# Kernel tuning notes

Measured on AMD Instinct MI355X. Metric: run time of the kernel, lower is better.

## Reference

```python
import jax, jax.numpy as jnp
import numpy as np

BITS = 4
GROUPSIZE = 128
IN_FEATURES = 4096
OUT_FEATURES = 11008
N_GROUPS = IN_FEATURES // GROUPSIZE  # 32
MASK = (1 << BITS) - 1  # 15


def setup_inputs() -> dict:
    key = jax.random.key(0)
    ks = jax.random.split(key, 5)
    x = jax.random.normal(ks[0], (2, 2048, IN_FEATURES), dtype=jnp.float32)
    qweight = jax.random.randint(ks[1], (IN_FEATURES // 8, OUT_FEATURES), 0, 2**31 - 1, dtype=jnp.int32)
    qzeros = jax.random.randint(ks[2], (N_GROUPS, OUT_FEATURES // 8), 0, 2**31 - 1, dtype=jnp.int32)
    scales = jax.random.uniform(ks[3], (N_GROUPS, OUT_FEATURES), dtype=jnp.float16)
    bias = jax.random.normal(ks[4], (OUT_FEATURES,), dtype=jnp.float32)
    return {"x": x, "qweight": qweight, "qzeros": qzeros, "scales": scales, "bias": bias}


def _dequant(qweight, qzeros, scales):
    # wf = [0, 4, 8, ..., 28]: bit offsets of the 8 int4 nibbles in each int32
    wf = jnp.arange(0, 32, BITS, dtype=jnp.int32)
    # unpack weights: [IN//8, OUT] -> [IN//8, 8, OUT] -> [N_GROUPS, GROUPSIZE, OUT]
    w = (qweight[:, None, :] >> wf[None, :, None]) & MASK
    w = w.reshape(N_GROUPS, GROUPSIZE, OUT_FEATURES).astype(jnp.float32)
    # unpack zeros: [NG, OUT//8] -> [NG, OUT//8, 8] -> [NG, 1, OUT]
    z = (qzeros[:, :, None] >> wf[None, None, :]) & MASK
    z = z.reshape(N_GROUPS, 1, OUT_FEATURES).astype(jnp.float32)
    s = scales.astype(jnp.float32)[:, None, :]  # [NG, 1, OUT]
    # scales * w - scales * z, per group; fused elementwise
    return (s * (w - z)).reshape(IN_FEATURES, OUT_FEATURES)


def reference(x, qweight, qzeros, scales, bias):
    W = _dequant(qweight, qzeros, scales)  # [IN, OUT] fp32
    out = jnp.matmul(x.astype(jnp.float32), W) + bias
    return out
```

## Files before the change

### kernel.cpp

```cpp
#include <hip/hip_runtime.h>
#include <hip/hip_fp16.h>

#define K_DIM 4096
#define N_DIM 11008
#define NZ8   1376
#define BM    256
#define BN    256
#define NT_N  43
#define NKT   64
#define ATB   32768

typedef _Float16 f16x8 __attribute__((ext_vector_type(8)));
typedef float    f32x4 __attribute__((ext_vector_type(4)));

#define SB()    __builtin_amdgcn_sched_barrier(0)
#define BAR()   __builtin_amdgcn_s_barrier()
#define VMW(N)  do { asm volatile("s_waitcnt vmcnt(" #N ")" ::: "memory"); SB(); } while (0)
#define LGKM0() do { asm volatile("s_waitcnt lgkmcnt(0)" ::: "memory"); SB(); } while (0)

__device__ __forceinline__ f16x8 dq8(unsigned q, __half2 scp, __half2 nzp)
{
    const unsigned mu = 0xE400E400u;
    const __half2 m1024 = *(const __half2*)&mu;
    union { __half2 h2[4]; f16x8 v; } p;
#pragma unroll
    for (int d = 0; d < 4; ++d) {
        unsigned t = ((q >> (4 * d)) & 0x000F000Fu) | 0x64006400u;
        p.h2[d] = __hfma2(__hadd2(*(const __half2*)&t, m1024), scp, nzp);
    }
    return p.v;
}

__global__ __launch_bounds__(256)
void r15_xcvt(const float* __restrict__ x, __half* __restrict__ xh, int nchunks)
{
    int c = blockIdx.x * 256 + threadIdx.x;
    const int stride = gridDim.x * 256;
    for (; c < nchunks; c += stride) {
        const int row = c & 255;
        const int sl  = (c >> 8) & 3;
        const int kh  = (c >> 10) & 1;
        const int tl  = c >> 11;
        const int mt  = tl >> 6;
        const int kt  = tl & 63;
        const size_t gm = (size_t)mt * 256 + row;
        const int kb = kt * 64 + kh * 32 + sl * 8;
        const float4 f0 = *(const float4*)(x + gm * K_DIM + kb);
        const float4 f1 = *(const float4*)(x + gm * K_DIM + kb + 4);
        union { __half2 h2[4]; int4 v; } p;
        p.h2[0] = __floats2half2_rn(f0.x, f1.x);
        p.h2[1] = __floats2half2_rn(f0.y, f1.y);
        p.h2[2] = __floats2half2_rn(f0.z, f1.z);
        p.h2[3] = __floats2half2_rn(f0.w, f1.w);
        ((int4*)xh)[c] = p.v;
    }
}

#define ISSUE_Q8(D0,D1,D2,D3,D4,D5,D6,D7) do { \
    asm volatile( \
        "global_load_dword %0, %8, off\n\t" \
        "global_load_dword %1, %8, off offset:64\n\t" \
        "global_load_dword %2, %8, off offset:128\n\t" \
        "global_load_dword %3, %8, off offset:192\n\t" \
        "global_load_dword %4, %9, off\n\t" \
        "global_load_dword %5, %9, off offset:64\n\t" \
        "global_load_dword %6, %9, off offset:128\n\t" \
        "global_load_dword %7, %9, off offset:192" \
        : "=&v"(D0), "=&v"(D1), "=&v"(D2), "=&v"(D3), \
          "=&v"(D4), "=&v"(D5), "=&v"(D6), "=&v"(D7) \
        : "v"(qp0), "v"(qp1) : "memory"); \
    qp0 += 8 * N_DIM; qp1 += 8 * N_DIM; \
} while (0)

#define ISSUE_SZ() do { \
    asm volatile( \
        "global_load_dword %0, %8, off\n\t" \
        "global_load_dword %1, %8, off offset:64\n\t" \
        "global_load_dword %2, %8, off offset:128\n\t" \
        "global_load_dword %3, %8, off offset:192\n\t" \
        "global_load_dword %4, %9, off\n\t" \
        "global_load_dword %5, %9, off offset:8\n\t" \
        "global_load_dword %6, %9, off offset:16\n\t" \
        "global_load_dword %7, %9, off offset:24" \
        : "=&v"(sS0), "=&v"(sS1), "=&v"(sS2), "=&v"(sS3), \
          "=&v"(sZ0), "=&v"(sZ1), "=&v"(sZ2), "=&v"(sZ3) \
        : "v"(sp), "v"(zp) : "memory"); \
    sp += N_DIM; zp += NZ8; \
} while (0)

#define ISSUE_A(BUFP, T) do { \
    const char* _s = agp + (size_t)(T) * ATB; \
    _Pragma("unroll") for (int j = 0; j < 4; ++j) \
        __builtin_amdgcn_global_load_lds((const unsigned int*)(_s + j * 8192), \
            (unsigned int*)((BUFP) + j * 8192 + tid * 16), 16, 0, 0); \
} while (0)

#define FRAGS(ARp, KH) do { \
    _Pragma("unroll") for (int m = 0; m < 8; ++m) \
        af[m] = *(const f16x8*)((ARp) + (KH) * 16384 + aOff + m * 256); \
} while (0)

#define DQ4(Q0,Q1,Q2,Q3) do { \
    bf[0] = dq8(Q0, scp0, nzp0); bf[1] = dq8(Q1, scp1, nzp1); \
    bf[2] = dq8(Q2, scp2, nzp2); bf[3] = dq8(Q3, scp3, nzp3); \
} while (0)

#define MFMA32() do { \
    __builtin_amdgcn_s_setprio(1); \
    _Pragma("unroll") for (int m = 0; m < 8; ++m) \
        _Pragma("unroll") for (int n = 0; n < 4; ++n) \
            acc[m][n] = __builtin_amdgcn_mfma_f32_16x16x32_f16(af[m], bf[n], acc[m][n], 0, 0, 0); \
    __builtin_amdgcn_s_setprio(0); \
    SB(); \
} while (0)

#define CVT_S() do { \
    const float _s0 = __uint_as_float(sS0), _s1 = __uint_as_float(sS1); \
    const float _s2 = __uint_as_float(sS2), _s3 = __uint_as_float(sS3); \
    const __half _h0 = __float2half_rn(_s0), _h1 = __float2half_rn(_s1); \
    const __half _h2 = __float2half_rn(_s2), _h3 = __float2half_rn(_s3); \
    scp0 = __half2(_h0, _h0); scp1 = __half2(_h1, _h1); \
    scp2 = __half2(_h2, _h2); scp3 = __half2(_h3, _h3); \
    const __half _n0 = __float2half_rn(-_s0 * (float)((sZ0 >> sh4) & 15u)); \
    const __half _n1 = __float2half_rn(-_s1 * (float)((sZ1 >> sh4) & 15u)); \
    const __half _n2 = __float2half_rn(-_s2 * (float)((sZ2 >> sh4) & 15u)); \
    const __half _n3 = __float2half_rn(-_s3 * (float)((sZ3 >> sh4) & 15u)); \
    nzp0 = __half2(_n0, _n0); nzp1 = __half2(_n1, _n1); \
    nzp2 = __half2(_n2, _n2); nzp3 = __half2(_n3, _n3); \
} while (0)

__global__ __launch_bounds__(512, 2)
void r15_gemm(const __half* __restrict__ xh,
              const int*   __restrict__ qweight,
              const int*   __restrict__ qzeros,
              const float* __restrict__ scales,
              const float* __restrict__ bias,
              float* __restrict__ out)
{
    __shared__ __align__(16) unsigned char A0s[ATB], A1s[ATB];

    const int tid  = threadIdx.x;
    const int lane = tid & 63;
    const int wid  = tid >> 6;
    const int wr   = (wid >> 2) * 128;
    const int wc   = (wid & 3) * 64;

    int bid = blockIdx.x;
    const int cpx = gridDim.x >> 3;
    bid = (bid & 7) * cpx + (bid >> 3);
    const int bm0 = (bid / NT_N) * BM;
    const int bn0 = (bid % NT_N) * BN;

    const int frow = lane & 15, kb8 = lane >> 4;
    const int ngl2 = bn0 + wc + frow;
    const int sh4  = (ngl2 & 7) * 4;
    const int aOff = kb8 * 4096 + (wr + frow) * 16;

    const char* agp = (const char*)xh + ((size_t)(bm0 >> 8) * NKT) * ATB + tid * 16;

    const int*   qp0 = qweight + (size_t)kb8 * N_DIM + ngl2;
    const int*   qp1 = qweight + (size_t)(kb8 + 4) * N_DIM + ngl2;
    const float* sp  = scales + (size_t)N_DIM + ngl2;
    const int*   zp  = qzeros + (size_t)NZ8 + (ngl2 >> 3);

    unsigned char *aR = A0s, *aW = A1s;

    f32x4 acc[8][4];
#pragma unroll
    for (int m = 0; m < 8; ++m)
#pragma unroll
        for (int n = 0; n < 4; ++n)
            acc[m][n] = (f32x4){0.f, 0.f, 0.f, 0.f};
    f16x8 af[8], bf[4];
    __half2 scp0, scp1, scp2, scp3, nzp0, nzp1, nzp2, nzp3;
    unsigned qa0, qa1, qa2, qa3, qa4, qa5, qa6, qa7;
    unsigned qb0, qb1, qb2, qb3, qb4, qb5, qb6, qb7;
    unsigned sS0, sS1, sS2, sS3, sZ0, sZ1, sZ2, sZ3;

    sS0 = __float_as_uint(scales[ngl2]);
    sS1 = __float_as_uint(scales[ngl2 + 16]);
    sS2 = __float_as_uint(scales[ngl2 + 32]);
    sS3 = __float_as_uint(scales[ngl2 + 48]);
    sZ0 = (unsigned)qzeros[(ngl2 >> 3) + 0];
    sZ1 = (unsigned)qzeros[(ngl2 >> 3) + 2];
    sZ2 = (unsigned)qzeros[(ngl2 >> 3) + 4];
    sZ3 = (unsigned)qzeros[(ngl2 >> 3) + 6];
    asm volatile("" : "+v"(sS0), "+v"(sS1), "+v"(sS2), "+v"(sS3),
                      "+v"(sZ0), "+v"(sZ1), "+v"(sZ2), "+v"(sZ3));
    VMW(0);
    ISSUE_Q8(qa0, qa1, qa2, qa3, qa4, qa5, qa6, qa7);
    ISSUE_A(aR, 0);
    ISSUE_Q8(qb0, qb1, qb2, qb3, qb4, qb5, qb6, qb7);
    ISSUE_A(aW, 1);
    VMW(12);
    BAR();

    for (int u = 0; u < 31; ++u) {
        const int t0 = 2 * u;
        CVT_S();
        FRAGS(aR, 0); DQ4(qa0, qa1, qa2, qa3); LGKM0(); MFMA32();
        FRAGS(aR, 1); DQ4(qa4, qa5, qa6, qa7);
        ISSUE_Q8(qa0, qa1, qa2, qa3, qa4, qa5, qa6, qa7);
        ISSUE_SZ();
        LGKM0(); MFMA32();
        VMW(16);
        BAR(); SB();
        { unsigned char* tp = aR; aR = aW; aW = tp; }
        ISSUE_A(aW, t0 + 2);
        FRAGS(aR, 0); DQ4(qb0, qb1, qb2, qb3); LGKM0(); MFMA32();
        FRAGS(aR, 1); DQ4(qb4, qb5, qb6, qb7);
        ISSUE_Q8(qb0, qb1, qb2, qb3, qb4, qb5, qb6, qb7);
        LGKM0(); MFMA32();
        VMW(8);
        BAR(); SB();
        { unsigned char* tp = aR; aR = aW; aW = tp; }
        ISSUE_A(aW, t0 + 3);
    }

    CVT_S();
    FRAGS(aR, 0); DQ4(qa0, qa1, qa2, qa3); LGKM0(); MFMA32();
    FRAGS(aR, 1); DQ4(qa4, qa5, qa6, qa7); LGKM0(); MFMA32();
    VMW(0);
    BAR(); SB();
    { unsigned char* tp = aR; aR = aW; aW = tp; }
    FRAGS(aR, 0); DQ4(qb0, qb1, qb2, qb3); LGKM0(); MFMA32();
    FRAGS(aR, 1); DQ4(qb4, qb5, qb6, qb7); LGKM0(); MFMA32();

    const int crow0 = (lane >> 4) << 2, ccol = lane & 15;
#pragma unroll
    for (int n = 0; n < 4; ++n) {
        const int col = bn0 + wc + n * 16 + ccol;
        const float bv = bias[col];
#pragma unroll
        for (int m = 0; m < 8; ++m) {
            const int row = bm0 + wr + m * 16 + crow0;
#pragma unroll
            for (int j = 0; j < 4; ++j)
                out[(size_t)(row + j) * N_DIM + col] = acc[m][n][j] + bv;
        }
    }
}

typedef __bf16 bf16x8 __attribute__((ext_vector_type(8)));

__global__ __launch_bounds__(256, 2)
void r15_fb(const float* __restrict__ x,
            const int*   __restrict__ qweight,
            const int*   __restrict__ qzeros,
            const float* __restrict__ scales,
            const float* __restrict__ bias,
            float* __restrict__ out)
{
    __shared__ __align__(16) unsigned char Asm[128 * 64 * 2];
    __shared__ __align__(16) unsigned char Bsm[128 * 64 * 2];
    const int tid = threadIdx.x, lane = tid & 63, wv = tid >> 6;
    const int wr = (wv >> 1) * 64, wc = (wv & 1) * 64;
    int bid = blockIdx.x;
    const int cpx = gridDim.x >> 3;
    bid = (bid & 7) * cpx + (bid >> 3);
    const int bm0 = (bid / 86) * 128, bn0 = (bid % 86) * 128;
    const int ar = tid >> 4, ac4 = tid & 15;
    const float* xp = x + (size_t)(bm0 + ar) * K_DIM + ac4 * 4;
    unsigned char* aw = Asm + ar * 128 + ((ac4 * 8) ^ ((ar & 7) << 4));
    const int bnn = tid & 127, bk8q = tid >> 7, ngl = bn0 + bnn;
    const int* qwp = qweight + (size_t)bk8q * N_DIM + ngl;
    unsigned char* bw = Bsm + bnn * 128;
    const int bsw = bnn & 7;
    const int frow = lane & 15, kb8 = lane >> 4, fsw = frow & 7;
    f32x4 acc[4][4];
#pragma unroll
    for (int m = 0; m < 4; ++m)
#pragma unroll
        for (int n = 0; n < 4; ++n) acc[m][n] = (f32x4){0.f, 0.f, 0.f, 0.f};
    float sc = 0.f, nsz = 0.f;
    for (int kt = 0; kt < K_DIM / 64; ++kt) {
        const int k0 = kt * 64;
        if ((k0 & 127) == 0) {
            const int g = k0 >> 7;
            sc = scales[(size_t)g * N_DIM + ngl];
            const unsigned zq = (unsigned)qzeros[(size_t)g * NZ8 + (ngl >> 3)];
            nsz = -sc * (float)((zq >> ((ngl & 7) * 4)) & 15u);
        }
#pragma unroll
        for (int i = 0; i < 8; ++i) {
            const float4 v = *(const float4*)(xp + (size_t)i * 16 * K_DIM + k0);
            union { __bf16 h[4]; unsigned long long u; } p;
            p.h[0] = (__bf16)v.x; p.h[1] = (__bf16)v.y;
            p.h[2] = (__bf16)v.z; p.h[3] = (__bf16)v.w;
            *(unsigned long long*)(aw + i * 16 * 128) = p.u;
        }
#pragma unroll
        for (int i = 0; i < 4; ++i) {
            const int k8 = 2 * i + bk8q;
            const unsigned q = (unsigned)qwp[(size_t)(kt * 8 + 2 * i) * N_DIM];
            union { __bf16 h[8]; bf16x8 v8; } p;
#pragma unroll
            for (int j = 0; j < 8; ++j)
                p.h[j] = (__bf16)__builtin_fmaf(sc, (float)((q >> (4 * j)) & 15u), nsz);
            *(bf16x8*)(bw + ((k8 ^ bsw) << 4)) = p.v8;
        }
        __syncthreads();
#pragma unroll
        for (int kh = 0; kh < 2; ++kh) {
            const int ksl = (kh << 2) + kb8;
            bf16x8 a2[4], b2[4];
#pragma unroll
            for (int m = 0; m < 4; ++m)
                a2[m] = *(const bf16x8*)(Asm + (wr + m * 16 + frow) * 128 + ((ksl ^ fsw) << 4));
#pragma unroll
            for (int n = 0; n < 4; ++n)
                b2[n] = *(const bf16x8*)(Bsm + (wc + n * 16 + frow) * 128 + ((ksl ^ fsw) << 4));
#pragma unroll
            for (int m = 0; m < 4; ++m)
#pragma unroll
                for (int n = 0; n < 4; ++n)
                    acc[m][n] = __builtin_amdgcn_mfma_f32_16x16x32_bf16(a2[m], b2[n], acc[m][n], 0, 0, 0);
        }
        __syncthreads();
    }
    const int crow0 = (lane >> 4) << 2, ccol = lane & 15;
#pragma unroll
    for (int n = 0; n < 4; ++n) {
        const int col = bn0 + wc + n * 16 + ccol;
        const float bv = bias[col];
#pragma unroll
        for (int m = 0; m < 4; ++m) {
            const int row = bm0 + wr + m * 16 + crow0;
#pragma unroll
            for (int j = 0; j < 4; ++j)
                out[(size_t)(row + j) * N_DIM + col] = acc[m][n][j] + bv;
        }
    }
}

extern "C" void kernel_launch(void* const* d_in, const int* in_sizes, int n_in,
                              void* d_out, int out_size, void* d_ws, size_t ws_size,
                              hipStream_t stream)
{
    const float* x   = (const float*)d_in[0];
    const int*   qw  = (const int*)d_in[1];
    const int*   qz  = (const int*)d_in[2];
    const float* scl = (const float*)d_in[3];
    const float* bs  = (const float*)d_in[4];
    float* out = (float*)d_out;

    const int M = in_sizes[0] / K_DIM;
    const size_t xh_bytes = (size_t)M * K_DIM * 2;

    if (ws_size >= xh_bytes) {
        __half* xh = (__half*)d_ws;
        const int nchunks = M * K_DIM / 8;
        hipLaunchKernelGGL(r15_xcvt, dim3(2048), dim3(256), 0, stream, x, xh, nchunks);
        dim3 grid((M / BM) * NT_N);
        hipLaunchKernelGGL(r15_gemm, grid, dim3(512), 0, stream,
                           xh, qw, qz, scl, bs, out);
    } else {
        dim3 grid((M / 128) * 86);
        hipLaunchKernelGGL(r15_fb, grid, dim3(256), 0, stream,
                           x, qw, qz, scl, bs, out);
    }
}
```

Measured before the change: 386.2 us.

## Switch GEMM to 32x32x16 MFMA with k-sliced A fragments and pipelined LDS reads

Replaces the 16x16x32 MFMA tiling with 32x32x16 MFMAs, so each wave holds 4x2 accumulators of 16 floats instead of 8x4 of 4. The x fp16 staging layout, the qweight/scale/zero load pattern and the dequant per lane change to match, and each lane now needs only two scale/zero pairs. A-fragment LDS reads are split into four k-slices and double-buffered across register sets with partial lgkmcnt waits, so LDS latency overlaps MFMA issue. The aim is fewer MFMA instructions, less dequant work per lane and fewer stalls on LDS, at the cost of a more intricate schedule and output row mapping.

```diff
diff --git a/kernel.cpp b/kernel.cpp
--- a/kernel.cpp
+++ b/kernel.cpp
@@ -10,13 +10,13 @@
 #define NKT   64
 #define ATB   32768
 
-typedef _Float16 f16x8 __attribute__((ext_vector_type(8)));
-typedef float    f32x4 __attribute__((ext_vector_type(4)));
-
-#define SB()    __builtin_amdgcn_sched_barrier(0)
-#define BAR()   __builtin_amdgcn_s_barrier()
-#define VMW(N)  do { asm volatile("s_waitcnt vmcnt(" #N ")" ::: "memory"); SB(); } while (0)
-#define LGKM0() do { asm volatile("s_waitcnt lgkmcnt(0)" ::: "memory"); SB(); } while (0)
+typedef _Float16 f16x8  __attribute__((ext_vector_type(8)));
+typedef float    f32x16 __attribute__((ext_vector_type(16)));
+
+#define SB()     __builtin_amdgcn_sched_barrier(0)
+#define BAR()    __builtin_amdgcn_s_barrier()
+#define VMW(N)   do { asm volatile("s_waitcnt vmcnt(" #N ")" ::: "memory"); SB(); } while (0)
+#define LGKMC(N) do { asm volatile("s_waitcnt lgkmcnt(" #N ")" ::: "memory"); SB(); } while (0)
 
 __device__ __forceinline__ f16x8 dq8(unsigned q, __half2 scp, __half2 nzp)
 {
@@ -32,19 +32,18 @@
 }
 
 __global__ __launch_bounds__(256)
-void r15_xcvt(const float* __restrict__ x, __half* __restrict__ xh, int nchunks)
+void r17_xcvt(const float* __restrict__ x, __half* __restrict__ xh, int nchunks)
 {
     int c = blockIdx.x * 256 + threadIdx.x;
     const int stride = gridDim.x * 256;
     for (; c < nchunks; c += stride) {
         const int row = c & 255;
-        const int sl  = (c >> 8) & 3;
-        const int kh  = (c >> 10) & 1;
+        const int ch  = (c >> 8) & 7;
         const int tl  = c >> 11;
         const int mt  = tl >> 6;
         const int kt  = tl & 63;
         const size_t gm = (size_t)mt * 256 + row;
-        const int kb = kt * 64 + kh * 32 + sl * 8;
+        const int kb = kt * 64 + ch * 8;
         const float4 f0 = *(const float4*)(x + gm * K_DIM + kb);
         const float4 f1 = *(const float4*)(x + gm * K_DIM + kb + 4);
         union { __half2 h2[4]; int4 v; } p;
@@ -59,31 +58,26 @@
 #define ISSUE_Q8(D0,D1,D2,D3,D4,D5,D6,D7) do { \
     asm volatile( \
         "global_load_dword %0, %8, off\n\t" \
-        "global_load_dword %1, %8, off offset:64\n\t" \
-        "global_load_dword %2, %8, off offset:128\n\t" \
-        "global_load_dword %3, %8, off offset:192\n\t" \
-        "global_load_dword %4, %9, off\n\t" \
-        "global_load_dword %5, %9, off offset:64\n\t" \
-        "global_load_dword %6, %9, off offset:128\n\t" \
-        "global_load_dword %7, %9, off offset:192" \
+        "global_load_dword %1, %8, off offset:128\n\t" \
+        "global_load_dword %2, %9, off\n\t" \
+        "global_load_dword %3, %9, off offset:128\n\t" \
+        "global_load_dword %4, %10, off\n\t" \
+        "global_load_dword %5, %10, off offset:128\n\t" \
+        "global_load_dword %6, %11, off\n\t" \
+        "global_load_dword %7, %11, off offset:128" \
         : "=&v"(D0), "=&v"(D1), "=&v"(D2), "=&v"(D3), \
           "=&v"(D4), "=&v"(D5), "=&v"(D6), "=&v"(D7) \
-        : "v"(qp0), "v"(qp1) : "memory"); \
-    qp0 += 8 * N_DIM; qp1 += 8 * N_DIM; \
+        : "v"(qp0), "v"(qp1), "v"(qp2), "v"(qp3) : "memory"); \
+    qp0 += 8 * N_DIM; qp1 += 8 * N_DIM; qp2 += 8 * N_DIM; qp3 += 8 * N_DIM; \
 } while (0)
 
 #define ISSUE_SZ() do { \
     asm volatile( \
-        "global_load_dword %0, %8, off\n\t" \
-        "global_load_dword %1, %8, off offset:64\n\t" \
-        "global_load_dword %2, %8, off offset:128\n\t" \
-        "global_load_dword %3, %8, off offset:192\n\t" \
-        "global_load_dword %4, %9, off\n\t" \
-        "global_load_dword %5, %9, off offset:8\n\t" \
-        "global_load_dword %6, %9, off offset:16\n\t" \
-        "global_load_dword %7, %9, off offset:24" \
-        : "=&v"(sS0), "=&v"(sS1), "=&v"(sS2), "=&v"(sS3), \
-          "=&v"(sZ0), "=&v"(sZ1), "=&v"(sZ2), "=&v"(sZ3) \
+        "global_load_dword %0, %4, off\n\t" \
+        "global_load_dword %1, %4, off offset:128\n\t" \
+        "global_load_dword %2, %5, off\n\t" \
+        "global_load_dword %3, %5, off offset:16" \
+        : "=&v"(sS0), "=&v"(sS1), "=&v"(sZ0), "=&v"(sZ1) \
         : "v"(sp), "v"(zp) : "memory"); \
     sp += N_DIM; zp += NZ8; \
 } while (0)
@@ -95,42 +89,38 @@
             (unsigned int*)((BUFP) + j * 8192 + tid * 16), 16, 0, 0); \
 } while (0)
 
-#define FRAGS(ARp, KH) do { \
-    _Pragma("unroll") for (int m = 0; m < 8; ++m) \
-        af[m] = *(const f16x8*)((ARp) + (KH) * 16384 + aOff + m * 256); \
-} while (0)
-
-#define DQ4(Q0,Q1,Q2,Q3) do { \
-    bf[0] = dq8(Q0, scp0, nzp0); bf[1] = dq8(Q1, scp1, nzp1); \
-    bf[2] = dq8(Q2, scp2, nzp2); bf[3] = dq8(Q3, scp3, nzp3); \
-} while (0)
-
-#define MFMA32() do { \
+#define FRAGS_KS(ARp, KS, DEST) do { \
+    _Pragma("unroll") for (int mb = 0; mb < 4; ++mb) \
+        DEST[mb] = *(const f16x8*)((ARp) + (KS) * 8192 + aBase + mb * 512); \
+} while (0)
+
+#define DQ2(Q0, Q1) do { \
+    bf0 = dq8(Q0, scp0, nzp0); bf1 = dq8(Q1, scp1, nzp1); \
+} while (0)
+
+#define MFMA8(AF) do { \
     __builtin_amdgcn_s_setprio(1); \
-    _Pragma("unroll") for (int m = 0; m < 8; ++m) \
-        _Pragma("unroll") for (int n = 0; n < 4; ++n) \
-            acc[m][n] = __builtin_amdgcn_mfma_f32_16x16x32_f16(af[m], bf[n], acc[m][n], 0, 0, 0); \
+    _Pragma("unroll") for (int mb = 0; mb < 4; ++mb) { \
+        acc[mb][0] = __builtin_amdgcn_mfma_f32_32x32x16_f16(AF[mb], bf0, acc[mb][0], 0, 0, 0); \
+        acc[mb][1] = __builtin_amdgcn_mfma_f32_32x32x16_f16(AF[mb], bf1, acc[mb][1], 0, 0, 0); \
+    } \
     __builtin_amdgcn_s_setprio(0); \
     SB(); \
 } while (0)
 
 #define CVT_S() do { \
     const float _s0 = __uint_as_float(sS0), _s1 = __uint_as_float(sS1); \
-    const float _s2 = __uint_as_float(sS2), _s3 = __uint_as_float(sS3); \
     const __half _h0 = __float2half_rn(_s0), _h1 = __float2half_rn(_s1); \
-    const __half _h2 = __float2half_rn(_s2), _h3 = __float2half_rn(_s3); \
     scp0 = __half2(_h0, _h0); scp1 = __half2(_h1, _h1); \
-    scp2 = __half2(_h2, _h2); scp3 = __half2(_h3, _h3); \
     const __half _n0 = __float2half_rn(-_s0 * (float)((sZ0 >> sh4) & 15u)); \
     const __half _n1 = __float2half_rn(-_s1 * (float)((sZ1 >> sh4) & 15u)); \
-    const __half _n2 = __float2half_rn(-_s2 * (float)((sZ2 >> sh4) & 15u)); \
-    const __half _n3 = __float2half_rn(-_s3 * (float)((sZ3 >> sh4) & 15u)); \
     nzp0 = __half2(_n0, _n0); nzp1 = __half2(_n1, _n1); \
-    nzp2 = __half2(_n2, _n2); nzp3 = __half2(_n3, _n3); \
-} while (0)
+} while (0)
+
+#define SWAP_A() do { unsigned char* _tp = aR; aR = aW; aW = _tp; } while (0)
 
 __global__ __launch_bounds__(512, 2)
-void r15_gemm(const __half* __restrict__ xh,
+void r17_gemm(const __half* __restrict__ xh,
               const int*   __restrict__ qweight,
               const int*   __restrict__ qzeros,
               const float* __restrict__ scales,
@@ -151,42 +141,42 @@
     const int bm0 = (bid / NT_N) * BM;
     const int bn0 = (bid % NT_N) * BN;
 
-    const int frow = lane & 15, kb8 = lane >> 4;
-    const int ngl2 = bn0 + wc + frow;
-    const int sh4  = (ngl2 & 7) * 4;
-    const int aOff = kb8 * 4096 + (wr + frow) * 16;
+    const int lrow = lane & 31;
+    const int hi   = lane >> 5;
+    const int colb = bn0 + wc + lrow;
+    const int sh4  = (colb & 7) * 4;
+    const int aBase = hi * 4096 + (wr + lrow) * 16;
 
     const char* agp = (const char*)xh + ((size_t)(bm0 >> 8) * NKT) * ATB + tid * 16;
 
-    const int*   qp0 = qweight + (size_t)kb8 * N_DIM + ngl2;
-    const int*   qp1 = qweight + (size_t)(kb8 + 4) * N_DIM + ngl2;
-    const float* sp  = scales + (size_t)N_DIM + ngl2;
-    const int*   zp  = qzeros + (size_t)NZ8 + (ngl2 >> 3);
+    const int* qp0 = qweight + (size_t)(0 + hi) * N_DIM + colb;
+    const int* qp1 = qweight + (size_t)(2 + hi) * N_DIM + colb;
+    const int* qp2 = qweight + (size_t)(4 + hi) * N_DIM + colb;
+    const int* qp3 = qweight + (size_t)(6 + hi) * N_DIM + colb;
+    const float* sp = scales + (size_t)N_DIM + colb;
+    const int*   zp = qzeros + (size_t)NZ8 + (colb >> 3);
 
     unsigned char *aR = A0s, *aW = A1s;
 
-    f32x4 acc[8][4];
-#pragma unroll
-    for (int m = 0; m < 8; ++m)
-#pragma unroll
-        for (int n = 0; n < 4; ++n)
-            acc[m][n] = (f32x4){0.f, 0.f, 0.f, 0.f};
-    f16x8 af[8], bf[4];
-    __half2 scp0, scp1, scp2, scp3, nzp0, nzp1, nzp2, nzp3;
+    f32x16 acc[4][2];
+#pragma unroll
+    for (int mb = 0; mb < 4; ++mb)
+#pragma unroll
+        for (int nb = 0; nb < 2; ++nb)
+#pragma unroll
+            for (int r = 0; r < 16; ++r) acc[mb][nb][r] = 0.f;
+
+    f16x8 afA[4], afB[4], bf0, bf1;
+    __half2 scp0, scp1, nzp0, nzp1;
     unsigned qa0, qa1, qa2, qa3, qa4, qa5, qa6, qa7;
     unsigned qb0, qb1, qb2, qb3, qb4, qb5, qb6, qb7;
-    unsigned sS0, sS1, sS2, sS3, sZ0, sZ1, sZ2, sZ3;
-
-    sS0 = __float_as_uint(scales[ngl2]);
-    sS1 = __float_as_uint(scales[ngl2 + 16]);
-    sS2 = __float_as_uint(scales[ngl2 + 32]);
-    sS3 = __float_as_uint(scales[ngl2 + 48]);
-    sZ0 = (unsigned)qzeros[(ngl2 >> 3) + 0];
-    sZ1 = (unsigned)qzeros[(ngl2 >> 3) + 2];
-    sZ2 = (unsigned)qzeros[(ngl2 >> 3) + 4];
-    sZ3 = (unsigned)qzeros[(ngl2 >> 3) + 6];
-    asm volatile("" : "+v"(sS0), "+v"(sS1), "+v"(sS2), "+v"(sS3),
-                      "+v"(sZ0), "+v"(sZ1), "+v"(sZ2), "+v"(sZ3));
+    unsigned sS0, sS1, sZ0, sZ1;
+
+    sS0 = __float_as_uint(scales[colb]);
+    sS1 = __float_as_uint(scales[colb + 32]);
+    sZ0 = (unsigned)qzeros[(colb >> 3)];
+    sZ1 = (unsigned)qzeros[(colb >> 3) + 4];
+    asm volatile("" : "+v"(sS0), "+v"(sS1), "+v"(sZ0), "+v"(sZ1));
     VMW(0);
     ISSUE_Q8(qa0, qa1, qa2, qa3, qa4, qa5, qa6, qa7);
     ISSUE_A(aR, 0);
@@ -194,57 +184,70 @@
     ISSUE_A(aW, 1);
     VMW(12);
     BAR();
+    FRAGS_KS(aR, 0, afA);
 
     for (int u = 0; u < 31; ++u) {
-        const int t0 = 2 * u;
         CVT_S();
-        FRAGS(aR, 0); DQ4(qa0, qa1, qa2, qa3); LGKM0(); MFMA32();
-        FRAGS(aR, 1); DQ4(qa4, qa5, qa6, qa7);
+        FRAGS_KS(aR, 1, afB); DQ2(qa0, qa1); LGKMC(4); MFMA8(afA);
+        FRAGS_KS(aR, 2, afA); DQ2(qa2, qa3); LGKMC(4); MFMA8(afB);
+        FRAGS_KS(aR, 3, afB); DQ2(qa4, qa5); LGKMC(4); MFMA8(afA);
+        DQ2(qa6, qa7);
         ISSUE_Q8(qa0, qa1, qa2, qa3, qa4, qa5, qa6, qa7);
         ISSUE_SZ();
-        LGKM0(); MFMA32();
-        VMW(16);
+        LGKMC(0); MFMA8(afB);
+        VMW(12);
         BAR(); SB();
-        { unsigned char* tp = aR; aR = aW; aW = tp; }
-        ISSUE_A(aW, t0 + 2);
-        FRAGS(aR, 0); DQ4(qb0, qb1, qb2, qb3); LGKM0(); MFMA32();
-        FRAGS(aR, 1); DQ4(qb4, qb5, qb6, qb7);
+        SWAP_A();
+        ISSUE_A(aW, 2 * u + 2);
+        FRAGS_KS(aR, 0, afA);
+        FRAGS_KS(aR, 1, afB); DQ2(qb0, qb1); LGKMC(4); MFMA8(afA);
+        FRAGS_KS(aR, 2, afA); DQ2(qb2, qb3); LGKMC(4); MFMA8(afB);
+        FRAGS_KS(aR, 3, afB); DQ2(qb4, qb5); LGKMC(4); MFMA8(afA);
+        DQ2(qb6, qb7);
         ISSUE_Q8(qb0, qb1, qb2, qb3, qb4, qb5, qb6, qb7);
-        LGKM0(); MFMA32();
+        LGKMC(0); MFMA8(afB);
         VMW(8);
         BAR(); SB();
-        { unsigned char* tp = aR; aR = aW; aW = tp; }
-        ISSUE_A(aW, t0 + 3);
+        SWAP_A();
+        ISSUE_A(aW, 2 * u + 3);
+        FRAGS_KS(aR, 0, afA);
     }
 
     CVT_S();
-    FRAGS(aR, 0); DQ4(qa0, qa1, qa2, qa3); LGKM0(); MFMA32();
-    FRAGS(aR, 1); DQ4(qa4, qa5, qa6, qa7); LGKM0(); MFMA32();
+    FRAGS_KS(aR, 1, afB); DQ2(qa0, qa1); LGKMC(4); MFMA8(afA);
+    FRAGS_KS(aR, 2, afA); DQ2(qa2, qa3); LGKMC(4); MFMA8(afB);
+    FRAGS_KS(aR, 3, afB); DQ2(qa4, qa5); LGKMC(4); MFMA8(afA);
+    DQ2(qa6, qa7); LGKMC(0); MFMA8(afB);
     VMW(0);
     BAR(); SB();
-    { unsigned char* tp = aR; aR = aW; aW = tp; }
-    FRAGS(aR, 0); DQ4(qb0, qb1, qb2, qb3); LGKM0(); MFMA32();
-    FRAGS(aR, 1); DQ4(qb4, qb5, qb6, qb7); LGKM0(); MFMA32();
-
-    const int crow0 = (lane >> 4) << 2, ccol = lane & 15;
-#pragma unroll
-    for (int n = 0; n < 4; ++n) {
-        const int col = bn0 + wc + n * 16 + ccol;
+    SWAP_A();
+    FRAGS_KS(aR, 0, afA);
+    FRAGS_KS(aR, 1, afB); DQ2(qb0, qb1); LGKMC(4); MFMA8(afA);
+    FRAGS_KS(aR, 2, afA); DQ2(qb2, qb3); LGKMC(4); MFMA8(afB);
+    FRAGS_KS(aR, 3, afB); DQ2(qb4, qb5); LGKMC(4); MFMA8(afA);
+    DQ2(qb6, qb7); LGKMC(0); MFMA8(afB);
+
+#pragma unroll
+    for (int nb = 0; nb < 2; ++nb) {
+        const int col = colb + nb * 32;
         const float bv = bias[col];
 #pragma unroll
-        for (int m = 0; m < 8; ++m) {
-            const int row = bm0 + wr + m * 16 + crow0;
-#pragma unroll
-            for (int j = 0; j < 4; ++j)
-                out[(size_t)(row + j) * N_DIM + col] = acc[m][n][j] + bv;
+        for (int mb = 0; mb < 4; ++mb) {
+            const int rb = bm0 + wr + mb * 32 + 4 * hi;
+#pragma unroll
+            for (int r = 0; r < 16; ++r) {
+                const int row = rb + (r & 3) + 8 * (r >> 2);
+                out[(size_t)row * N_DIM + col] = acc[mb][nb][r] + bv;
+            }
         }
     }
 }
 
 typedef __bf16 bf16x8 __attribute__((ext_vector_type(8)));
+typedef float  f32x4  __attribute__((ext_vector_type(4)));
 
 __global__ __launch_bounds__(256, 2)
-void r15_fb(const float* __restrict__ x,
+void r17_fb(const float* __restrict__ x,
             const int*   __restrict__ qweight,
             const int*   __restrict__ qzeros,
             const float* __restrict__ scales,
@@ -350,13 +353,13 @@
     if (ws_size >= xh_bytes) {
         __half* xh = (__half*)d_ws;
         const int nchunks = M * K_DIM / 8;
-        hipLaunchKernelGGL(r15_xcvt, dim3(2048), dim3(256), 0, stream, x, xh, nchunks);
+        hipLaunchKernelGGL(r17_xcvt, dim3(2048), dim3(256), 0, stream, x, xh, nchunks);
         dim3 grid((M / BM) * NT_N);
-        hipLaunchKernelGGL(r15_gemm, grid, dim3(512), 0, stream,
+        hipLaunchKernelGGL(r17_gemm, grid, dim3(512), 0, stream,
                            xh, qw, qz, scl, bs, out);
     } else {
         dim3 grid((M / 128) * 86);
-        hipLaunchKernelGGL(r15_fb, grid, dim3(256), 0, stream,
+        hipLaunchKernelGGL(r17_fb, grid, dim3(256), 0, stream,
                            x, qw, qz, scl, bs, out);
     }
 }
```

Result: slower. 415.5 us (+7.6%).

## Software-pipeline LDS A-fragment loads with MFMA using double-buffered fragment registers

Applied to the files above, without the earlier changes.

Splits each 8x4 MFMA block into two 4x4 halves with separate low/high accumulators and two A-fragment register sets. The LDS reads for the next half are issued before the MFMAs on the current half, and the explicit lgkmcnt(0) waits are removed, so LDS latency is meant to hide behind matrix work. The last half-tile's MFMAs are carried across the barrier into the next tile. This raises register pressure from the extra fragment set and depends on the compiler inserting correct waits.

```diff
diff --git a/kernel.cpp b/kernel.cpp
--- a/kernel.cpp
+++ b/kernel.cpp
@@ -16,7 +16,6 @@
 #define SB()    __builtin_amdgcn_sched_barrier(0)
 #define BAR()   __builtin_amdgcn_s_barrier()
 #define VMW(N)  do { asm volatile("s_waitcnt vmcnt(" #N ")" ::: "memory"); SB(); } while (0)
-#define LGKM0() do { asm volatile("s_waitcnt lgkmcnt(0)" ::: "memory"); SB(); } while (0)
 
 __device__ __forceinline__ f16x8 dq8(unsigned q, __half2 scp, __half2 nzp)
 {
@@ -32,7 +31,7 @@
 }
 
 __global__ __launch_bounds__(256)
-void r15_xcvt(const float* __restrict__ x, __half* __restrict__ xh, int nchunks)
+void r19_xcvt(const float* __restrict__ x, __half* __restrict__ xh, int nchunks)
 {
     int c = blockIdx.x * 256 + threadIdx.x;
     const int stride = gridDim.x * 256;
@@ -95,9 +94,10 @@
             (unsigned int*)((BUFP) + j * 8192 + tid * 16), 16, 0, 0); \
 } while (0)
 
-#define FRAGS(ARp, KH) do { \
-    _Pragma("unroll") for (int m = 0; m < 8; ++m) \
-        af[m] = *(const f16x8*)((ARp) + (KH) * 16384 + aOff + m * 256); \
+#define FRISS(BUFP, KH, MH, DEST) do { \
+    _Pragma("unroll") for (int i = 0; i < 4; ++i) \
+        DEST[i] = *(const f16x8*)((BUFP) + (KH) * 16384 + aOff + (MH) * 1024 + i * 256); \
+    SB(); \
 } while (0)
 
 #define DQ4(Q0,Q1,Q2,Q3) do { \
@@ -105,11 +105,11 @@
     bf[2] = dq8(Q2, scp2, nzp2); bf[3] = dq8(Q3, scp3, nzp3); \
 } while (0)
 
-#define MFMA32() do { \
+#define MFMA16(AF) do { \
     __builtin_amdgcn_s_setprio(1); \
-    _Pragma("unroll") for (int m = 0; m < 8; ++m) \
+    _Pragma("unroll") for (int m = 0; m < 4; ++m) \
         _Pragma("unroll") for (int n = 0; n < 4; ++n) \
-            acc[m][n] = __builtin_amdgcn_mfma_f32_16x16x32_f16(af[m], bf[n], acc[m][n], 0, 0, 0); \
+            accp[m][n] = __builtin_amdgcn_mfma_f32_16x16x32_f16(AF[m], bf[n], accp[m][n], 0, 0, 0); \
     __builtin_amdgcn_s_setprio(0); \
     SB(); \
 } while (0)
@@ -129,8 +129,19 @@
     nzp2 = __half2(_n2, _n2); nzp3 = __half2(_n3, _n3); \
 } while (0)
 
+#define SWAP_A() do { unsigned char* _tp = aR; aR = aW; aW = _tp; } while (0)
+
+#define TILE_CORE(QL0,QL1,QL2,QL3,QH0,QH1,QH2,QH3) do { \
+    FRISS(aR, 0, 1, afB);  DQ4(QL0, QL1, QL2, QL3); \
+    { auto& accp = accL; MFMA16(afA); } \
+    FRISS(aR, 1, 0, afA); \
+    { auto& accp = accH; MFMA16(afB); } \
+    FRISS(aR, 1, 1, afB);  DQ4(QH0, QH1, QH2, QH3); \
+    { auto& accp = accL; MFMA16(afA); } \
+} while (0)
+
 __global__ __launch_bounds__(512, 2)
-void r15_gemm(const __half* __restrict__ xh,
+void r19_gemm(const __half* __restrict__ xh,
               const int*   __restrict__ qweight,
               const int*   __restrict__ qzeros,
               const float* __restrict__ scales,
@@ -165,13 +176,15 @@
 
     unsigned char *aR = A0s, *aW = A1s;
 
-    f32x4 acc[8][4];
-#pragma unroll
-    for (int m = 0; m < 8; ++m)
-#pragma unroll
-        for (int n = 0; n < 4; ++n)
-            acc[m][n] = (f32x4){0.f, 0.f, 0.f, 0.f};
-    f16x8 af[8], bf[4];
+    f32x4 accL[4][4], accH[4][4];
+#pragma unroll
+    for (int m = 0; m < 4; ++m)
+#pragma unroll
+        for (int n = 0; n < 4; ++n) {
+            accL[m][n] = (f32x4){0.f, 0.f, 0.f, 0.f};
+            accH[m][n] = (f32x4){0.f, 0.f, 0.f, 0.f};
+        }
+    f16x8 afA[4], afB[4], bf[4];
     __half2 scp0, scp1, scp2, scp3, nzp0, nzp1, nzp2, nzp3;
     unsigned qa0, qa1, qa2, qa3, qa4, qa5, qa6, qa7;
     unsigned qb0, qb1, qb2, qb3, qb4, qb5, qb6, qb7;
@@ -194,37 +207,41 @@
     ISSUE_A(aW, 1);
     VMW(12);
     BAR();
+    FRISS(aR, 0, 0, afA);
 
     for (int u = 0; u < 31; ++u) {
         const int t0 = 2 * u;
         CVT_S();
-        FRAGS(aR, 0); DQ4(qa0, qa1, qa2, qa3); LGKM0(); MFMA32();
-        FRAGS(aR, 1); DQ4(qa4, qa5, qa6, qa7);
+        TILE_CORE(qa0, qa1, qa2, qa3, qa4, qa5, qa6, qa7);
         ISSUE_Q8(qa0, qa1, qa2, qa3, qa4, qa5, qa6, qa7);
         ISSUE_SZ();
-        LGKM0(); MFMA32();
+        SB();
         VMW(16);
-        BAR(); SB();
-        { unsigned char* tp = aR; aR = aW; aW = tp; }
-        ISSUE_A(aW, t0 + 2);
-        FRAGS(aR, 0); DQ4(qb0, qb1, qb2, qb3); LGKM0(); MFMA32();
-        FRAGS(aR, 1); DQ4(qb4, qb5, qb6, qb7);
+        BAR();
+        SWAP_A();
+        ISSUE_A(aW, t0 + 2); SB();
+        FRISS(aR, 0, 0, afA);
+        { auto& accp = accH; MFMA16(afB); }
+        TILE_CORE(qb0, qb1, qb2, qb3, qb4, qb5, qb6, qb7);
         ISSUE_Q8(qb0, qb1, qb2, qb3, qb4, qb5, qb6, qb7);
-        LGKM0(); MFMA32();
+        SB();
         VMW(8);
-        BAR(); SB();
-        { unsigned char* tp = aR; aR = aW; aW = tp; }
-        ISSUE_A(aW, t0 + 3);
+        BAR();
+        SWAP_A();
+        ISSUE_A(aW, t0 + 3); SB();
+        FRISS(aR, 0, 0, afA);
+        { auto& accp = accH; MFMA16(afB); }
     }
 
     CVT_S();
-    FRAGS(aR, 0); DQ4(qa0, qa1, qa2, qa3); LGKM0(); MFMA32();
-    FRAGS(aR, 1); DQ4(qa4, qa5, qa6, qa7); LGKM0(); MFMA32();
+    TILE_CORE(qa0, qa1, qa2, qa3, qa4, qa5, qa6, qa7);
     VMW(0);
-    BAR(); SB();
-    { unsigned char* tp = aR; aR = aW; aW = tp; }
-    FRAGS(aR, 0); DQ4(qb0, qb1, qb2, qb3); LGKM0(); MFMA32();
-    FRAGS(aR, 1); DQ4(qb4, qb5, qb6, qb7); LGKM0(); MFMA32();
+    BAR();
+    SWAP_A();
+    FRISS(aR, 0, 0, afA);
+    { auto& accp = accH; MFMA16(afB); }
+    TILE_CORE(qb0, qb1, qb2, qb3, qb4, qb5, qb6, qb7);
+    { auto& accp = accH; MFMA16(afB); }
 
     const int crow0 = (lane >> 4) << 2, ccol = lane & 15;
 #pragma unroll
@@ -232,11 +249,14 @@
         const int col = bn0 + wc + n * 16 + ccol;
         const float bv = bias[col];
 #pragma unroll
-        for (int m = 0; m < 8; ++m) {
-            const int row = bm0 + wr + m * 16 + crow0;
-#pragma unroll
-            for (int j = 0; j < 4; ++j)
-                out[(size_t)(row + j) * N_DIM + col] = acc[m][n][j] + bv;
+        for (int m = 0; m < 4; ++m) {
+            const int rowL = bm0 + wr + m * 16 + crow0;
+            const int rowH = rowL + 64;
+#pragma unroll
+            for (int j = 0; j < 4; ++j) {
+                out[(size_t)(rowL + j) * N_DIM + col] = accL[m][n][j] + bv;
+                out[(size_t)(rowH + j) * N_DIM + col] = accH[m][n][j] + bv;
+            }
         }
     }
 }
@@ -244,7 +264,7 @@
 typedef __bf16 bf16x8 __attribute__((ext_vector_type(8)));
 
 __global__ __launch_bounds__(256, 2)
-void r15_fb(const float* __restrict__ x,
+void r19_fb(const float* __restrict__ x,
             const int*   __restrict__ qweight,
             const int*   __restrict__ qzeros,
             const float* __restrict__ scales,
@@ -350,13 +370,13 @@
     if (ws_size >= xh_bytes) {
         __half* xh = (__half*)d_ws;
         const int nchunks = M * K_DIM / 8;
-        hipLaunchKernelGGL(r15_xcvt, dim3(2048), dim3(256), 0, stream, x, xh, nchunks);
+        hipLaunchKernelGGL(r19_xcvt, dim3(2048), dim3(256), 0, stream, x, xh, nchunks);
         dim3 grid((M / BM) * NT_N);
-        hipLaunchKernelGGL(r15_gemm, grid, dim3(512), 0, stream,
+        hipLaunchKernelGGL(r19_gemm, grid, dim3(512), 0, stream,
                            xh, qw, qz, scl, bs, out);
     } else {
         dim3 grid((M / 128) * 86);
-        hipLaunchKernelGGL(r15_fb, grid, dim3(256), 0, stream,
+        hipLaunchKernelGGL(r19_fb, grid, dim3(256), 0, stream,
                            x, qw, qz, scl, bs, out);
     }
 }
```

After: 403.2 us. +4.4%, slower.

## Replace LDS-staged 256x256 tiles with register-direct 64x256 tiles, no barriers

Applied to the files above, without the earlier changes.

The GEMM tile shrinks from 256x256 with 8 waves to 64x256 with 4 waves. Each wave loads its A fragments straight from global memory into registers using dwordx4 loads, which drops the LDS double buffer, the LDS fragment reads and the block barriers. The x conversion kernel changes its packing to the 64-row fragment layout, and launch bounds change to allow 3 blocks per CU. In exchange, each dequantized weight fragment is now reused across only 64 rows instead of 256, so weight traffic and dequant work per output rise about fourfold.

```diff
diff --git a/kernel.cpp b/kernel.cpp
--- a/kernel.cpp
+++ b/kernel.cpp
@@ -4,19 +4,14 @@
 #define K_DIM 4096
 #define N_DIM 11008
 #define NZ8   1376
-#define BM    256
-#define BN    256
+#define NKT   64
 #define NT_N  43
-#define NKT   64
-#define ATB   32768
 
 typedef _Float16 f16x8 __attribute__((ext_vector_type(8)));
 typedef float    f32x4 __attribute__((ext_vector_type(4)));
 
 #define SB()    __builtin_amdgcn_sched_barrier(0)
-#define BAR()   __builtin_amdgcn_s_barrier()
 #define VMW(N)  do { asm volatile("s_waitcnt vmcnt(" #N ")" ::: "memory"); SB(); } while (0)
-#define LGKM0() do { asm volatile("s_waitcnt lgkmcnt(0)" ::: "memory"); SB(); } while (0)
 
 __device__ __forceinline__ f16x8 dq8(unsigned q, __half2 scp, __half2 nzp)
 {
@@ -32,18 +27,18 @@
 }
 
 __global__ __launch_bounds__(256)
-void r15_xcvt(const float* __restrict__ x, __half* __restrict__ xh, int nchunks)
+void r20_xcvt(const float* __restrict__ x, __half* __restrict__ xh, int nchunks)
 {
     int c = blockIdx.x * 256 + threadIdx.x;
     const int stride = gridDim.x * 256;
     for (; c < nchunks; c += stride) {
-        const int row = c & 255;
-        const int sl  = (c >> 8) & 3;
-        const int kh  = (c >> 10) & 1;
-        const int tl  = c >> 11;
+        const int row = c & 63;
+        const int sl  = (c >> 6) & 3;
+        const int kh  = (c >> 8) & 1;
+        const int tl  = c >> 9;
         const int mt  = tl >> 6;
         const int kt  = tl & 63;
-        const size_t gm = (size_t)mt * 256 + row;
+        const size_t gm = (size_t)mt * 64 + row;
         const int kb = kt * 64 + kh * 32 + sl * 8;
         const float4 f0 = *(const float4*)(x + gm * K_DIM + kb);
         const float4 f1 = *(const float4*)(x + gm * K_DIM + kb + 4);
@@ -56,20 +51,24 @@
     }
 }
 
-#define ISSUE_Q8(D0,D1,D2,D3,D4,D5,D6,D7) do { \
+#define ISSUE_A4(D, P) do { \
     asm volatile( \
-        "global_load_dword %0, %8, off\n\t" \
-        "global_load_dword %1, %8, off offset:64\n\t" \
-        "global_load_dword %2, %8, off offset:128\n\t" \
-        "global_load_dword %3, %8, off offset:192\n\t" \
-        "global_load_dword %4, %9, off\n\t" \
-        "global_load_dword %5, %9, off offset:64\n\t" \
-        "global_load_dword %6, %9, off offset:128\n\t" \
-        "global_load_dword %7, %9, off offset:192" \
-        : "=&v"(D0), "=&v"(D1), "=&v"(D2), "=&v"(D3), \
-          "=&v"(D4), "=&v"(D5), "=&v"(D6), "=&v"(D7) \
-        : "v"(qp0), "v"(qp1) : "memory"); \
-    qp0 += 8 * N_DIM; qp1 += 8 * N_DIM; \
+        "global_load_dwordx4 %0, %4, off\n\t" \
+        "global_load_dwordx4 %1, %4, off offset:256\n\t" \
+        "global_load_dwordx4 %2, %4, off offset:512\n\t" \
+        "global_load_dwordx4 %3, %4, off offset:768" \
+        : "=&v"(D[0]), "=&v"(D[1]), "=&v"(D[2]), "=&v"(D[3]) \
+        : "v"(P) : "memory"); \
+} while (0)
+
+#define ISSUE_Q4(D0,D1,D2,D3, P) do { \
+    asm volatile( \
+        "global_load_dword %0, %4, off\n\t" \
+        "global_load_dword %1, %4, off offset:64\n\t" \
+        "global_load_dword %2, %4, off offset:128\n\t" \
+        "global_load_dword %3, %4, off offset:192" \
+        : "=&v"(D0), "=&v"(D1), "=&v"(D2), "=&v"(D3) \
+        : "v"(P) : "memory"); \
 } while (0)
 
 #define ISSUE_SZ() do { \
@@ -88,28 +87,16 @@
     sp += N_DIM; zp += NZ8; \
 } while (0)
 
-#define ISSUE_A(BUFP, T) do { \
-    const char* _s = agp + (size_t)(T) * ATB; \
-    _Pragma("unroll") for (int j = 0; j < 4; ++j) \
-        __builtin_amdgcn_global_load_lds((const unsigned int*)(_s + j * 8192), \
-            (unsigned int*)((BUFP) + j * 8192 + tid * 16), 16, 0, 0); \
-} while (0)
-
-#define FRAGS(ARp, KH) do { \
-    _Pragma("unroll") for (int m = 0; m < 8; ++m) \
-        af[m] = *(const f16x8*)((ARp) + (KH) * 16384 + aOff + m * 256); \
-} while (0)
-
 #define DQ4(Q0,Q1,Q2,Q3) do { \
     bf[0] = dq8(Q0, scp0, nzp0); bf[1] = dq8(Q1, scp1, nzp1); \
     bf[2] = dq8(Q2, scp2, nzp2); bf[3] = dq8(Q3, scp3, nzp3); \
 } while (0)
 
-#define MFMA32() do { \
+#define MFMA16(AF) do { \
     __builtin_amdgcn_s_setprio(1); \
-    _Pragma("unroll") for (int m = 0; m < 8; ++m) \
+    _Pragma("unroll") for (int m = 0; m < 4; ++m) \
         _Pragma("unroll") for (int n = 0; n < 4; ++n) \
-            acc[m][n] = __builtin_amdgcn_mfma_f32_16x16x32_f16(af[m], bf[n], acc[m][n], 0, 0, 0); \
+            acc[m][n] = __builtin_amdgcn_mfma_f32_16x16x32_f16(AF[m], bf[n], acc[m][n], 0, 0, 0); \
     __builtin_amdgcn_s_setprio(0); \
     SB(); \
 } while (0)
@@ -129,52 +116,46 @@
     nzp2 = __half2(_n2, _n2); nzp3 = __half2(_n3, _n3); \
 } while (0)
 
-__global__ __launch_bounds__(512, 2)
-void r15_gemm(const __half* __restrict__ xh,
+__global__ __launch_bounds__(256, 3)
+void r20_gemm(const __half* __restrict__ xh,
               const int*   __restrict__ qweight,
               const int*   __restrict__ qzeros,
               const float* __restrict__ scales,
               const float* __restrict__ bias,
               float* __restrict__ out)
 {
-    __shared__ __align__(16) unsigned char A0s[ATB], A1s[ATB];
-
     const int tid  = threadIdx.x;
     const int lane = tid & 63;
     const int wid  = tid >> 6;
-    const int wr   = (wid >> 2) * 128;
-    const int wc   = (wid & 3) * 64;
 
     int bid = blockIdx.x;
     const int cpx = gridDim.x >> 3;
     bid = (bid & 7) * cpx + (bid >> 3);
-    const int bm0 = (bid / NT_N) * BM;
-    const int bn0 = (bid % NT_N) * BN;
+    const int mt = bid / NT_N;
+    const int nb = bid % NT_N;
 
     const int frow = lane & 15, kb8 = lane >> 4;
-    const int ngl2 = bn0 + wc + frow;
+    const int n0   = nb * 256 + wid * 64;
+    const int ngl2 = n0 + frow;
     const int sh4  = (ngl2 & 7) * 4;
-    const int aOff = kb8 * 4096 + (wr + frow) * 16;
-
-    const char* agp = (const char*)xh + ((size_t)(bm0 >> 8) * NKT) * ATB + tid * 16;
+
+    const char* ap = (const char*)xh + (size_t)mt * NKT * 8192
+                   + kb8 * 1024 + frow * 16;
 
     const int*   qp0 = qweight + (size_t)kb8 * N_DIM + ngl2;
-    const int*   qp1 = qweight + (size_t)(kb8 + 4) * N_DIM + ngl2;
+    const int*   qp1 = qweight + (size_t)(4 + kb8) * N_DIM + ngl2;
     const float* sp  = scales + (size_t)N_DIM + ngl2;
     const int*   zp  = qzeros + (size_t)NZ8 + (ngl2 >> 3);
 
-    unsigned char *aR = A0s, *aW = A1s;
-
-    f32x4 acc[8][4];
-#pragma unroll
-    for (int m = 0; m < 8; ++m)
+    f32x4 acc[4][4];
+#pragma unroll
+    for (int m = 0; m < 4; ++m)
 #pragma unroll
         for (int n = 0; n < 4; ++n)
             acc[m][n] = (f32x4){0.f, 0.f, 0.f, 0.f};
-    f16x8 af[8], bf[4];
+    f16x8 afA[4], afB[4], bf[4];
     __half2 scp0, scp1, scp2, scp3, nzp0, nzp1, nzp2, nzp3;
-    unsigned qa0, qa1, qa2, qa3, qa4, qa5, qa6, qa7;
-    unsigned qb0, qb1, qb2, qb3, qb4, qb5, qb6, qb7;
+    unsigned q0, q1, q2, q3, q4, q5, q6, q7;
     unsigned sS0, sS1, sS2, sS3, sZ0, sZ1, sZ2, sZ3;
 
     sS0 = __float_as_uint(scales[ngl2]);
@@ -188,55 +169,68 @@
     asm volatile("" : "+v"(sS0), "+v"(sS1), "+v"(sS2), "+v"(sS3),
                       "+v"(sZ0), "+v"(sZ1), "+v"(sZ2), "+v"(sZ3));
     VMW(0);
-    ISSUE_Q8(qa0, qa1, qa2, qa3, qa4, qa5, qa6, qa7);
-    ISSUE_A(aR, 0);
-    ISSUE_Q8(qb0, qb1, qb2, qb3, qb4, qb5, qb6, qb7);
-    ISSUE_A(aW, 1);
-    VMW(12);
-    BAR();
-
-    for (int u = 0; u < 31; ++u) {
-        const int t0 = 2 * u;
+    ISSUE_A4(afA, ap);
+    ISSUE_Q4(q0, q1, q2, q3, qp0);
+    ISSUE_A4(afB, ap + 4096);
+    ISSUE_Q4(q4, q5, q6, q7, qp1);
+    SB();
+    ap += 8192; qp0 += 8 * N_DIM; qp1 += 8 * N_DIM;
+
+    for (int g = 0; g < 31; ++g) {
+        VMW(8);
         CVT_S();
-        FRAGS(aR, 0); DQ4(qa0, qa1, qa2, qa3); LGKM0(); MFMA32();
-        FRAGS(aR, 1); DQ4(qa4, qa5, qa6, qa7);
-        ISSUE_Q8(qa0, qa1, qa2, qa3, qa4, qa5, qa6, qa7);
-        ISSUE_SZ();
-        LGKM0(); MFMA32();
+        DQ4(q0, q1, q2, q3);
+        MFMA16(afA);
+        ISSUE_A4(afA, ap); SB();
+        ISSUE_Q4(q0, q1, q2, q3, qp0); SB();
+        VMW(8);
+        DQ4(q4, q5, q6, q7);
+        MFMA16(afB);
+        ISSUE_A4(afB, ap + 4096); SB();
+        ISSUE_Q4(q4, q5, q6, q7, qp1);
+        ISSUE_SZ(); SB();
+        ap += 8192; qp0 += 8 * N_DIM; qp1 += 8 * N_DIM;
         VMW(16);
-        BAR(); SB();
-        { unsigned char* tp = aR; aR = aW; aW = tp; }
-        ISSUE_A(aW, t0 + 2);
-        FRAGS(aR, 0); DQ4(qb0, qb1, qb2, qb3); LGKM0(); MFMA32();
-        FRAGS(aR, 1); DQ4(qb4, qb5, qb6, qb7);
-        ISSUE_Q8(qb0, qb1, qb2, qb3, qb4, qb5, qb6, qb7);
-        LGKM0(); MFMA32();
-        VMW(8);
-        BAR(); SB();
-        { unsigned char* tp = aR; aR = aW; aW = tp; }
-        ISSUE_A(aW, t0 + 3);
-    }
-
+        DQ4(q0, q1, q2, q3);
+        MFMA16(afA);
+        ISSUE_A4(afA, ap); SB();
+        ISSUE_Q4(q0, q1, q2, q3, qp0); SB();
+        VMW(16);
+        DQ4(q4, q5, q6, q7);
+        MFMA16(afB);
+        ISSUE_A4(afB, ap + 4096); SB();
+        ISSUE_Q4(q4, q5, q6, q7, qp1); SB();
+        ap += 8192; qp0 += 8 * N_DIM; qp1 += 8 * N_DIM;
+    }
+
+    VMW(8);
     CVT_S();
-    FRAGS(aR, 0); DQ4(qa0, qa1, qa2, qa3); LGKM0(); MFMA32();
-    FRAGS(aR, 1); DQ4(qa4, qa5, qa6, qa7); LGKM0(); MFMA32();
+    DQ4(q0, q1, q2, q3);
+    MFMA16(afA);
+    ISSUE_A4(afA, ap); SB();
+    ISSUE_Q4(q0, q1, q2, q3, qp0); SB();
+    VMW(8);
+    DQ4(q4, q5, q6, q7);
+    MFMA16(afB);
+    ISSUE_A4(afB, ap + 4096); SB();
+    ISSUE_Q4(q4, q5, q6, q7, qp1); SB();
+    VMW(8);
+    DQ4(q0, q1, q2, q3);
+    MFMA16(afA);
     VMW(0);
-    BAR(); SB();
-    { unsigned char* tp = aR; aR = aW; aW = tp; }
-    FRAGS(aR, 0); DQ4(qb0, qb1, qb2, qb3); LGKM0(); MFMA32();
-    FRAGS(aR, 1); DQ4(qb4, qb5, qb6, qb7); LGKM0(); MFMA32();
-
-    const int crow0 = (lane >> 4) << 2, ccol = lane & 15;
+    DQ4(q4, q5, q6, q7);
+    MFMA16(afB);
+
 #pragma unroll
     for (int n = 0; n < 4; ++n) {
-        const int col = bn0 + wc + n * 16 + ccol;
+        const int col = n0 + n * 16 + frow;
         const float bv = bias[col];
 #pragma unroll
-        for (int m = 0; m < 8; ++m) {
-            const int row = bm0 + wr + m * 16 + crow0;
+        for (int m = 0; m < 4; ++m) {
+            const int row0 = mt * 64 + m * 16 + kb8 * 4;
 #pragma unroll
             for (int j = 0; j < 4; ++j)
-                out[(size_t)(row + j) * N_DIM + col] = acc[m][n][j] + bv;
+                out[(size_t)(row0 + j) * N_DIM + col] = acc[m][n][j] + bv;
         }
     }
 }
@@ -244,7 +238,7 @@
 typedef __bf16 bf16x8 __attribute__((ext_vector_type(8)));
 
 __global__ __launch_bounds__(256, 2)
-void r15_fb(const float* __restrict__ x,
+void r20_fb(const float* __restrict__ x,
             const int*   __restrict__ qweight,
             const int*   __restrict__ qzeros,
             const float* __restrict__ scales,
@@ -350,13 +344,13 @@
     if (ws_size >= xh_bytes) {
         __half* xh = (__half*)d_ws;
         const int nchunks = M * K_DIM / 8;
-        hipLaunchKernelGGL(r15_xcvt, dim3(2048), dim3(256), 0, stream, x, xh, nchunks);
-        dim3 grid((M / BM) * NT_N);
-        hipLaunchKernelGGL(r15_gemm, grid, dim3(512), 0, stream,
+        hipLaunchKernelGGL(r20_xcvt, dim3(2048), dim3(256), 0, stream, x, xh, nchunks);
+        dim3 grid((M / 64) * NT_N);
+        hipLaunchKernelGGL(r20_gemm, grid, dim3(256), 0, stream,
                            xh, qw, qz, scl, bs, out);
     } else {
         dim3 grid((M / 128) * 86);
-        hipLaunchKernelGGL(r15_fb, grid, dim3(256), 0, stream,
+        hipLaunchKernelGGL(r20_fb, grid, dim3(256), 0, stream,
                            x, qw, qz, scl, bs, out);
     }
 }
```

New measurement: 423.3 us. +9.6%, slower.
